# Kernel optimization log

Hardware: AMD Instinct MI355X
Metric: run time of the kernel (lower is better)

## Reference

```python
import jax, jax.numpy as jnp
import numpy as np

N_NODES = 50000
N_EDGES = 800000
IN_CH = 128
OUT_CH = 64
H1, C1 = 8, 8            # conv1: heads=8, out=8, concat -> 64
H2, C2 = 1, OUT_CH       # conv2: heads=1, out=64, concat=False
NEG_SLOPE = 0.2


def gat_conv(x, src, dst, W, att_src, att_dst, bias, heads, ch, concat):
    """PyG GATConv (self loops assumed already appended to src/dst).
    x: [N, F_in], W: [F_in, heads*ch], att_*: [heads, ch], bias: [heads*ch] or [ch]."""
    N = x.shape[0]
    h = (x @ W).reshape(N, heads, ch)                       # [N,H,C]
    a_s = jnp.einsum('nhc,hc->nh', h, att_src)              # [N,H]
    a_d = jnp.einsum('nhc,hc->nh', h, att_dst)              # [N,H]
    e = jax.nn.leaky_relu(a_s[src] + a_d[dst], NEG_SLOPE)   # [E,H]
    # segment softmax over incoming edges of each destination node
    m = jax.ops.segment_max(e, dst, num_segments=N)         # [N,H]
    ex = jnp.exp(e - m[dst])
    s = jax.ops.segment_sum(ex, dst, num_segments=N)        # [N,H]
    alpha = ex / (s[dst] + 1e-16)                           # [E,H]
    out = jax.ops.segment_sum(h[src] * alpha[:, :, None], dst, num_segments=N)  # [N,H,C]
    out = out.reshape(N, heads * ch) if concat else out.mean(axis=1)
    return out + bias


def setup_inputs() -> dict:
    key = jax.random.key(0)
    ks = jax.random.split(key, 12)
    glorot = lambda k, shape: jax.random.normal(k, shape, jnp.float32) * np.sqrt(2.0 / (shape[0] + shape[-1]))
    x = jax.random.normal(ks[0], (N_NODES, IN_CH), jnp.float32)
    edge_index = jax.random.randint(ks[1], (2, N_EDGES), 0, N_NODES, jnp.int64 if jax.config.read('jax_enable_x64') else jnp.int32).astype(jnp.int32)
    W1 = glorot(ks[2], (IN_CH, H1 * C1))
    att_src1 = glorot(ks[3], (H1, C1))
    att_dst1 = glorot(ks[4], (H1, C1))
    b1 = jnp.zeros((H1 * C1,), jnp.float32)
    W2 = glorot(ks[5], (H1 * C1, H2 * C2))
    att_src2 = glorot(ks[6], (H2, C2))
    att_dst2 = glorot(ks[7], (H2, C2))
    b2 = jnp.zeros((C2,), jnp.float32)
    return {"x": x, "edge_index": edge_index, "W1": W1, "att_src1": att_src1,
            "att_dst1": att_dst1, "b1": b1, "W2": W2, "att_src2": att_src2,
            "att_dst2": att_dst2, "b2": b2}


def reference(x, edge_index, W1, att_src1, att_dst1, b1, W2, att_src2, att_dst2, b2):
    N = x.shape[0]
    loops = jnp.arange(N, dtype=edge_index.dtype)
    src = jnp.concatenate([edge_index[0], loops])  # add_self_loops=True (PyG default)
    dst = jnp.concatenate([edge_index[1], loops])
    h = gat_conv(x, src, dst, W1, att_src1, att_dst1, b1, H1, C1, concat=True)
    h = jax.nn.elu(h)
    # F.dropout(training=self.training): identity in eval mode
    out = gat_conv(h, src, dst, W2, att_src2, att_dst2, b2, H2, C2, concat=False)
    return out
```

## Files before the change

kernel.cpp:

```cpp
#include <hip/hip_runtime.h>

#define NN 50000
#define NE 800000
#define NEG_SLOPE 0.2f

__device__ __forceinline__ float lrelu(float v) { return v > 0.f ? v : NEG_SLOPE * v; }
__device__ __forceinline__ unsigned short f2bf(float f) {
    unsigned u = __float_as_uint(f);
    return (unsigned short)((u + 0x7FFFu + ((u >> 16) & 1u)) >> 16);
}
__device__ __forceinline__ float rlane(float v, int l) {
    return __int_as_float(__builtin_amdgcn_readlane(__float_as_int(v), l));
}

__global__ __launch_bounds__(256) void setup(const float* __restrict__ W1,
                                             const float* __restrict__ W2,
                                             const float* __restrict__ as2,
                                             const float* __restrict__ ad2,
                                             int4* __restrict__ deg4,
                                             int* __restrict__ gcursor,
                                             float* __restrict__ W1S,
                                             float* __restrict__ W2S,
                                             float* __restrict__ w_as2,
                                             float* __restrict__ w_ad2) {
    int gid = blockIdx.x * 256 + threadIdx.x;
    if (gid < 12500) deg4[gid] = make_int4(0, 0, 0, 0);
    if (gid == 0) *gcursor = 0;
    if (gid < 8192) {
        int k = gid >> 6, c = gid & 63;
        W1S[((k >> 2) * 64 + c) * 4 + (k & 3)] = W1[k * 64 + c];
    } else if (gid < 12288) {
        int t = gid - 8192;
        int k = t >> 6, c = t & 63;
        W2S[((k >> 2) * 64 + c) * 4 + (k & 3)] = W2[k * 64 + c];
    }
    if (gid < 64) {
        float s = 0.f;
        for (int c = 0; c < 64; ++c) s += W2[gid * 64 + c] * as2[c];
        w_as2[gid] = s;
    } else if (gid < 128) {
        int k = gid - 64;
        float s = 0.f;
        for (int c = 0; c < 64; ++c) s += W2[k * 64 + c] * ad2[c];
        w_ad2[k] = s;
    }
}

__global__ __launch_bounds__(256) void hist_gemm1(const int* __restrict__ ei,
                                                  int* __restrict__ deg,
                                                  int* __restrict__ rank,
                                                  const float* __restrict__ x,
                                                  const float* __restrict__ W1S,
                                                  const float* __restrict__ att_s,
                                                  const float* __restrict__ att_d,
                                                  unsigned short* __restrict__ h1b,
                                                  float* __restrict__ a_s,
                                                  float2* __restrict__ nd1) {
    if (blockIdx.x < 3125) {
        int e = blockIdx.x * 256 + threadIdx.x;
        if (e < NE) rank[e] = atomicAdd(&deg[ei[NE + e]], 1);
        return;
    }
    int lane = threadIdx.x & 63;
    int wv   = __builtin_amdgcn_readfirstlane(threadIdx.x >> 6);
    int n0   = (blockIdx.x - 3125) * 16 + wv * 4;
    const float* __restrict__ xr = x + (size_t)n0 * 128;
    const float4* __restrict__ wp = (const float4*)W1S;
    float4 acc = {0.f, 0.f, 0.f, 0.f};
#pragma unroll 4
    for (int k4 = 0; k4 < 32; ++k4) {
        float4 w = wp[k4 * 64 + lane];
        const float* xk = xr + k4 * 4;
        acc.x += xk[0]   * w.x + xk[1]   * w.y + xk[2]   * w.z + xk[3]   * w.w;
        acc.y += xk[128] * w.x + xk[129] * w.y + xk[130] * w.z + xk[131] * w.w;
        acc.z += xk[256] * w.x + xk[257] * w.y + xk[258] * w.z + xk[259] * w.w;
        acc.w += xk[384] * w.x + xk[385] * w.y + xk[386] * w.z + xk[387] * w.w;
    }
    float as_l = att_s[lane], ad_l = att_d[lane];
    float av[4] = {acc.x, acc.y, acc.z, acc.w};
#pragma unroll
    for (int r = 0; r < 4; ++r) {
        float a = av[r];
        h1b[(size_t)(n0 + r) * 64 + lane] = f2bf(a);
        float ps = a * as_l, pd = a * ad_l;
        ps += __shfl_xor(ps, 1, 64); pd += __shfl_xor(pd, 1, 64);
        ps += __shfl_xor(ps, 2, 64); pd += __shfl_xor(pd, 2, 64);
        ps += __shfl_xor(ps, 4, 64); pd += __shfl_xor(pd, 4, 64);
        if ((lane & 7) == 0) {
            int h = lane >> 3;
            a_s[(n0 + r) * 8 + h] = ps;
            nd1[(n0 + r) * 8 + h] = make_float2(pd, lrelu(ps + pd));
        }
    }
}

__global__ __launch_bounds__(256) void scanA(const int* __restrict__ deg,
                                             int* __restrict__ offs,
                                             int* __restrict__ gcursor) {
    __shared__ int tmp[256];
    __shared__ int base;
    int i = blockIdx.x * 256 + threadIdx.x;
    int v = (i < NN) ? deg[i] : 0;
    tmp[threadIdx.x] = v;
    __syncthreads();
    for (int o = 1; o < 256; o <<= 1) {
        int t = (threadIdx.x >= o) ? tmp[threadIdx.x - o] : 0;
        __syncthreads();
        tmp[threadIdx.x] += t;
        __syncthreads();
    }
    if (threadIdx.x == 255) base = atomicAdd(gcursor, tmp[255]);
    __syncthreads();
    if (i < NN) offs[i] = base + tmp[threadIdx.x] - v;
}

__global__ void scatter(const int* __restrict__ ei, const int* __restrict__ rank,
                        const int* __restrict__ offs, int* __restrict__ srclist) {
    int e = blockIdx.x * blockDim.x + threadIdx.x;
    if (e < NE) {
        int d = ei[NE + e];
        srclist[offs[d] + rank[e]] = ei[e];
    }
}

__global__ __launch_bounds__(256) void agg1(const int* __restrict__ srclist,
                                            const int* __restrict__ offs,
                                            const int* __restrict__ degv,
                                            const float* __restrict__ a_s,
                                            const float2* __restrict__ nd1,
                                            const unsigned short* __restrict__ h1b,
                                            const float* __restrict__ b1,
                                            const float* __restrict__ w_as2,
                                            const float* __restrict__ w_ad2,
                                            unsigned short* __restrict__ xhb,
                                            float* __restrict__ a_s2,
                                            float2* __restrict__ nd2) {
    int wv   = threadIdx.x >> 6;
    int lane = threadIdx.x & 63;
    int d    = blockIdx.x * 4 + wv;
    int base = offs[d], dg = degv[d];
    int sub  = lane >> 3, hch = lane & 7;
    float2 nd = nd1[d * 8 + hch];
    float acc0 = 0.f, acc1 = 0.f, acc2 = 0.f, acc3 = 0.f;
    float acc4 = 0.f, acc5 = 0.f, acc6 = 0.f, acc7 = 0.f;
    float sm = 0.f;
    int k = sub;
    int s0 = 0, s1 = 0;
    float as0 = 0.f;
    uint4 hv0 = make_uint4(0, 0, 0, 0);
    if (k < dg)     s0 = srclist[base + k];
    if (k + 8 < dg) s1 = srclist[base + k + 8];
    if (k < dg) {
        as0 = a_s[s0 * 8 + hch];
        hv0 = *(const uint4*)&h1b[(size_t)s0 * 64 + hch * 8];
    }
    for (; k < dg; k += 8) {
        int   s2  = (k + 16 < dg) ? srclist[base + k + 16] : 0;
        float as1 = 0.f;
        uint4 hv1 = make_uint4(0, 0, 0, 0);
        if (k + 8 < dg) {
            as1 = a_s[s1 * 8 + hch];
            hv1 = *(const uint4*)&h1b[(size_t)s1 * 64 + hch * 8];
        }
        float ex = __expf(lrelu(as0 + nd.x) - nd.y);
        acc0 += __uint_as_float(hv0.x << 16)          * ex;
        acc1 += __uint_as_float(hv0.x & 0xffff0000u)  * ex;
        acc2 += __uint_as_float(hv0.y << 16)          * ex;
        acc3 += __uint_as_float(hv0.y & 0xffff0000u)  * ex;
        acc4 += __uint_as_float(hv0.z << 16)          * ex;
        acc5 += __uint_as_float(hv0.z & 0xffff0000u)  * ex;
        acc6 += __uint_as_float(hv0.w << 16)          * ex;
        acc7 += __uint_as_float(hv0.w & 0xffff0000u)  * ex;
        sm += ex;
        s0 = s1; s1 = s2; as0 = as1; hv0 = hv1;
    }
    if (sub == 0) {
        uint4 hv = *(const uint4*)&h1b[(size_t)d * 64 + hch * 8];
        acc0 += __uint_as_float(hv.x << 16);
        acc1 += __uint_as_float(hv.x & 0xffff0000u);
        acc2 += __uint_as_float(hv.y << 16);
        acc3 += __uint_as_float(hv.y & 0xffff0000u);
        acc4 += __uint_as_float(hv.z << 16);
        acc5 += __uint_as_float(hv.z & 0xffff0000u);
        acc6 += __uint_as_float(hv.w << 16);
        acc7 += __uint_as_float(hv.w & 0xffff0000u);
        sm += 1.f;
    }
#pragma unroll
    for (int m = 8; m < 64; m <<= 1) {
        acc0 += __shfl_xor(acc0, m, 64); acc1 += __shfl_xor(acc1, m, 64);
        acc2 += __shfl_xor(acc2, m, 64); acc3 += __shfl_xor(acc3, m, 64);
        acc4 += __shfl_xor(acc4, m, 64); acc5 += __shfl_xor(acc5, m, 64);
        acc6 += __shfl_xor(acc6, m, 64); acc7 += __shfl_xor(acc7, m, 64);
        sm   += __shfl_xor(sm, m, 64);
    }
    float inv = 1.f / sm;
    int li = (lane & 7) * 8;
    float4 bl = *(const float4*)&b1[li];
    float4 bh = *(const float4*)&b1[li + 4];
    float4 lo, hi;
    lo.x = acc0 * inv + bl.x; lo.x = lo.x > 0.f ? lo.x : expm1f(lo.x);
    lo.y = acc1 * inv + bl.y; lo.y = lo.y > 0.f ? lo.y : expm1f(lo.y);
    lo.z = acc2 * inv + bl.z; lo.z = lo.z > 0.f ? lo.z : expm1f(lo.z);
    lo.w = acc3 * inv + bl.w; lo.w = lo.w > 0.f ? lo.w : expm1f(lo.w);
    hi.x = acc4 * inv + bh.x; hi.x = hi.x > 0.f ? hi.x : expm1f(hi.x);
    hi.y = acc5 * inv + bh.y; hi.y = hi.y > 0.f ? hi.y : expm1f(hi.y);
    hi.z = acc6 * inv + bh.z; hi.z = hi.z > 0.f ? hi.z : expm1f(hi.z);
    hi.w = acc7 * inv + bh.w; hi.w = hi.w > 0.f ? hi.w : expm1f(hi.w);
    if (lane < 8) {
        uint4 pk;
        pk.x = ((unsigned)f2bf(lo.y) << 16) | f2bf(lo.x);
        pk.y = ((unsigned)f2bf(lo.w) << 16) | f2bf(lo.z);
        pk.z = ((unsigned)f2bf(hi.y) << 16) | f2bf(hi.x);
        pk.w = ((unsigned)f2bf(hi.w) << 16) | f2bf(hi.z);
        *(uint4*)&xhb[(size_t)d * 64 + lane * 8] = pk;
    }
    float4 s0v = *(const float4*)&w_as2[li], s1v = *(const float4*)&w_as2[li + 4];
    float4 d0v = *(const float4*)&w_ad2[li], d1v = *(const float4*)&w_ad2[li + 4];
    float ps = lo.x*s0v.x + lo.y*s0v.y + lo.z*s0v.z + lo.w*s0v.w
             + hi.x*s1v.x + hi.y*s1v.y + hi.z*s1v.z + hi.w*s1v.w;
    float pd = lo.x*d0v.x + lo.y*d0v.y + lo.z*d0v.z + lo.w*d0v.w
             + hi.x*d1v.x + hi.y*d1v.y + hi.z*d1v.z + hi.w*d1v.w;
    ps += __shfl_xor(ps, 1, 64); pd += __shfl_xor(pd, 1, 64);
    ps += __shfl_xor(ps, 2, 64); pd += __shfl_xor(pd, 2, 64);
    ps += __shfl_xor(ps, 4, 64); pd += __shfl_xor(pd, 4, 64);
    if (lane == 0) {
        a_s2[d] = ps;
        nd2[d]  = make_float2(pd, lrelu(ps + pd));
    }
}

__global__ __launch_bounds__(256) void agg2(const int* __restrict__ srclist,
                                            const int* __restrict__ offs,
                                            const int* __restrict__ degv,
                                            const float* __restrict__ a_s2,
                                            const float2* __restrict__ nd2,
                                            const unsigned short* __restrict__ xhb,
                                            const float* __restrict__ W2S,
                                            const float* __restrict__ b2,
                                            float* __restrict__ out) {
    int wv   = threadIdx.x >> 6;
    int lane = threadIdx.x & 63;
    int d    = blockIdx.x * 4 + wv;
    int base = offs[d], dg = degv[d];
    int sub  = lane >> 3, hch = lane & 7;
    float2 nd = nd2[d];
    float acc0 = 0.f, acc1 = 0.f, acc2 = 0.f, acc3 = 0.f;
    float acc4 = 0.f, acc5 = 0.f, acc6 = 0.f, acc7 = 0.f;
    float sm = 0.f;
    int k = sub;
    int s0 = 0, s1 = 0;
    float as0 = 0.f;
    uint4 hv0 = make_uint4(0, 0, 0, 0);
    if (k < dg)     s0 = srclist[base + k];
    if (k + 8 < dg) s1 = srclist[base + k + 8];
    if (k < dg) {
        as0 = a_s2[s0];
        hv0 = *(const uint4*)&xhb[(size_t)s0 * 64 + hch * 8];
    }
    for (; k < dg; k += 8) {
        int   s2  = (k + 16 < dg) ? srclist[base + k + 16] : 0;
        float as1 = 0.f;
        uint4 hv1 = make_uint4(0, 0, 0, 0);
        if (k + 8 < dg) {
            as1 = a_s2[s1];
            hv1 = *(const uint4*)&xhb[(size_t)s1 * 64 + hch * 8];
        }
        float ex = __expf(lrelu(as0 + nd.x) - nd.y);
        acc0 += __uint_as_float(hv0.x << 16)          * ex;
        acc1 += __uint_as_float(hv0.x & 0xffff0000u)  * ex;
        acc2 += __uint_as_float(hv0.y << 16)          * ex;
        acc3 += __uint_as_float(hv0.y & 0xffff0000u)  * ex;
        acc4 += __uint_as_float(hv0.z << 16)          * ex;
        acc5 += __uint_as_float(hv0.z & 0xffff0000u)  * ex;
        acc6 += __uint_as_float(hv0.w << 16)          * ex;
        acc7 += __uint_as_float(hv0.w & 0xffff0000u)  * ex;
        sm += ex;
        s0 = s1; s1 = s2; as0 = as1; hv0 = hv1;
    }
    if (sub == 0) {
        uint4 hv = *(const uint4*)&xhb[(size_t)d * 64 + hch * 8];
        acc0 += __uint_as_float(hv.x << 16);
        acc1 += __uint_as_float(hv.x & 0xffff0000u);
        acc2 += __uint_as_float(hv.y << 16);
        acc3 += __uint_as_float(hv.y & 0xffff0000u);
        acc4 += __uint_as_float(hv.z << 16);
        acc5 += __uint_as_float(hv.z & 0xffff0000u);
        acc6 += __uint_as_float(hv.w << 16);
        acc7 += __uint_as_float(hv.w & 0xffff0000u);
        sm += 1.f;
    }
#pragma unroll
    for (int m = 8; m < 64; m <<= 1) {
        acc0 += __shfl_xor(acc0, m, 64); acc1 += __shfl_xor(acc1, m, 64);
        acc2 += __shfl_xor(acc2, m, 64); acc3 += __shfl_xor(acc3, m, 64);
        acc4 += __shfl_xor(acc4, m, 64); acc5 += __shfl_xor(acc5, m, 64);
        acc6 += __shfl_xor(acc6, m, 64); acc7 += __shfl_xor(acc7, m, 64);
        sm   += __shfl_xor(sm, m, 64);
    }
    float inv = 1.f / sm;
    float t0 = acc0 * inv, t1 = acc1 * inv, t2 = acc2 * inv, t3 = acc3 * inv;
    float t4 = acc4 * inv, t5 = acc5 * inv, t6 = acc6 * inv, t7 = acc7 * inv;
    const float4* wp = (const float4*)W2S;
    float o = 0.f;
#pragma unroll
    for (int k4 = 0; k4 < 16; ++k4) {
        float4 w = wp[k4 * 64 + lane];
        int j = k4 >> 1;
        if (k4 & 1)
            o += rlane(t4, j) * w.x + rlane(t5, j) * w.y + rlane(t6, j) * w.z + rlane(t7, j) * w.w;
        else
            o += rlane(t0, j) * w.x + rlane(t1, j) * w.y + rlane(t2, j) * w.z + rlane(t3, j) * w.w;
    }
    out[(size_t)d * 64 + lane] = o + b2[lane];
}

extern "C" void kernel_launch(void* const* d_in, const int* in_sizes, int n_in,
                              void* d_out, int out_size, void* d_ws, size_t ws_size,
                              hipStream_t stream) {
    const float* x   = (const float*)d_in[0];
    const int*   ei  = (const int*)d_in[1];
    const float* W1  = (const float*)d_in[2];
    const float* as1 = (const float*)d_in[3];
    const float* ad1 = (const float*)d_in[4];
    const float* b1  = (const float*)d_in[5];
    const float* W2  = (const float*)d_in[6];
    const float* as2 = (const float*)d_in[7];
    const float* ad2 = (const float*)d_in[8];
    const float* b2  = (const float*)d_in[9];
    float* out = (float*)d_out;

    float* ws = (float*)d_ws;
    unsigned short* h1b = (unsigned short*)ws;
    unsigned short* xhb = (unsigned short*)(ws + 1600000);
    float*  a_s1 = ws + 3200000;
    float2* nd1  = (float2*)(ws + 3600000);
    float*  a_s2 = ws + 4400000;
    float2* nd2  = (float2*)(ws + 4450000);
    int* deg     = (int*)(ws + 4550000);
    int* offs    = deg + 50000;
    int* gcursor = offs + 50000;
    int* rank    = gcursor + 64;
    int* srclist = rank + 800000;
    float* W1S   = (float*)(srclist + 800000);
    float* W2S   = W1S + 8192;
    float* w_as2 = W2S + 4096;
    float* w_ad2 = w_as2 + 64;

    setup<<<49, 256, 0, stream>>>(W1, W2, as2, ad2, (int4*)deg, gcursor,
                                  W1S, W2S, w_as2, w_ad2);
    hist_gemm1<<<6250, 256, 0, stream>>>(ei, deg, rank, x, W1S, as1, ad1,
                                         h1b, a_s1, nd1);
    scanA<<<196, 256, 0, stream>>>(deg, offs, gcursor);
    scatter<<<3125, 256, 0, stream>>>(ei, rank, offs, srclist);

    agg1<<<12500, 256, 0, stream>>>(srclist, offs, deg, a_s1, nd1, h1b, b1,
                                    w_as2, w_ad2, xhb, a_s2, nd2);
    agg2<<<12500, 256, 0, stream>>>(srclist, offs, deg, a_s2, nd2, xhb, W2S, b2, out);
}
```

Before: 160.4 us.

## Split histogram out of GEMM and fuse CSR scatter with layer-1 GEMM

Moves the degree histogram into its own kernel that handles four strided edges per thread, and merges the CSR scatter into the layer-1 GEMM kernel. The scatter and GEMM now run as different block ranges of one launch, with each scatter thread also handling four edges. The aim is to cut per-thread launch and scheduling overhead on the small atomic and scatter passes and let the scatter overlap the GEMM. In exchange the GEMM no longer overlaps the histogram atomics, so the histogram now runs alone before the scan.

```diff
diff --git a/kernel.cpp b/kernel.cpp
--- a/kernel.cpp
+++ b/kernel.cpp
@@ -3,6 +3,7 @@
 #define NN 50000
 #define NE 800000
 #define NEG_SLOPE 0.2f
+#define S4 200192
 
 __device__ __forceinline__ float lrelu(float v) { return v > 0.f ? v : NEG_SLOPE * v; }
 __device__ __forceinline__ unsigned short f2bf(float f) {
@@ -46,24 +47,77 @@
     }
 }
 
-__global__ __launch_bounds__(256) void hist_gemm1(const int* __restrict__ ei,
-                                                  int* __restrict__ deg,
-                                                  int* __restrict__ rank,
-                                                  const float* __restrict__ x,
-                                                  const float* __restrict__ W1S,
-                                                  const float* __restrict__ att_s,
-                                                  const float* __restrict__ att_d,
-                                                  unsigned short* __restrict__ h1b,
-                                                  float* __restrict__ a_s,
-                                                  float2* __restrict__ nd1) {
-    if (blockIdx.x < 3125) {
-        int e = blockIdx.x * 256 + threadIdx.x;
-        if (e < NE) rank[e] = atomicAdd(&deg[ei[NE + e]], 1);
+__global__ __launch_bounds__(256) void hist4(const int* __restrict__ ei,
+                                             int* __restrict__ deg,
+                                             int* __restrict__ rank) {
+    int tid = blockIdx.x * 256 + threadIdx.x;
+    int e0 = tid, e1 = tid + S4, e2 = tid + 2 * S4, e3 = tid + 3 * S4;
+    bool p3 = e3 < NE;
+    int d0 = ei[NE + e0];
+    int d1 = ei[NE + e1];
+    int d2 = ei[NE + e2];
+    int d3 = p3 ? ei[NE + e3] : 0;
+    int r0 = atomicAdd(&deg[d0], 1);
+    int r1 = atomicAdd(&deg[d1], 1);
+    int r2 = atomicAdd(&deg[d2], 1);
+    int r3 = p3 ? atomicAdd(&deg[d3], 1) : 0;
+    rank[e0] = r0;
+    rank[e1] = r1;
+    rank[e2] = r2;
+    if (p3) rank[e3] = r3;
+}
+
+__global__ __launch_bounds__(256) void scanA(const int* __restrict__ deg,
+                                             int* __restrict__ offs,
+                                             int* __restrict__ gcursor) {
+    __shared__ int tmp[256];
+    __shared__ int base;
+    int i = blockIdx.x * 256 + threadIdx.x;
+    int v = (i < NN) ? deg[i] : 0;
+    tmp[threadIdx.x] = v;
+    __syncthreads();
+    for (int o = 1; o < 256; o <<= 1) {
+        int t = (threadIdx.x >= o) ? tmp[threadIdx.x - o] : 0;
+        __syncthreads();
+        tmp[threadIdx.x] += t;
+        __syncthreads();
+    }
+    if (threadIdx.x == 255) base = atomicAdd(gcursor, tmp[255]);
+    __syncthreads();
+    if (i < NN) offs[i] = base + tmp[threadIdx.x] - v;
+}
+
+__global__ __launch_bounds__(256) void scatter_gemm1(const int* __restrict__ ei,
+                                                     const int* __restrict__ rank,
+                                                     const int* __restrict__ offs,
+                                                     int* __restrict__ srclist,
+                                                     const float* __restrict__ x,
+                                                     const float* __restrict__ W1S,
+                                                     const float* __restrict__ att_s,
+                                                     const float* __restrict__ att_d,
+                                                     unsigned short* __restrict__ h1b,
+                                                     float* __restrict__ a_s,
+                                                     float2* __restrict__ nd1) {
+    if (blockIdx.x < 782) {
+        int tid = blockIdx.x * 256 + threadIdx.x;
+        int e0 = tid, e1 = tid + S4, e2 = tid + 2 * S4, e3 = tid + 3 * S4;
+        bool p3 = e3 < NE;
+        int s0 = ei[e0], d0 = ei[NE + e0], r0 = rank[e0];
+        int s1 = ei[e1], d1 = ei[NE + e1], r1 = rank[e1];
+        int s2 = ei[e2], d2 = ei[NE + e2], r2 = rank[e2];
+        int s3 = 0, d3 = 0, r3 = 0;
+        if (p3) { s3 = ei[e3]; d3 = ei[NE + e3]; r3 = rank[e3]; }
+        int o0 = offs[d0], o1 = offs[d1], o2 = offs[d2];
+        int o3 = p3 ? offs[d3] : 0;
+        srclist[o0 + r0] = s0;
+        srclist[o1 + r1] = s1;
+        srclist[o2 + r2] = s2;
+        if (p3) srclist[o3 + r3] = s3;
         return;
     }
     int lane = threadIdx.x & 63;
     int wv   = __builtin_amdgcn_readfirstlane(threadIdx.x >> 6);
-    int n0   = (blockIdx.x - 3125) * 16 + wv * 4;
+    int n0   = (blockIdx.x - 782) * 16 + wv * 4;
     const float* __restrict__ xr = x + (size_t)n0 * 128;
     const float4* __restrict__ wp = (const float4*)W1S;
     float4 acc = {0.f, 0.f, 0.f, 0.f};
@@ -91,35 +145,6 @@
             a_s[(n0 + r) * 8 + h] = ps;
             nd1[(n0 + r) * 8 + h] = make_float2(pd, lrelu(ps + pd));
         }
-    }
-}
-
-__global__ __launch_bounds__(256) void scanA(const int* __restrict__ deg,
-                                             int* __restrict__ offs,
-                                             int* __restrict__ gcursor) {
-    __shared__ int tmp[256];
-    __shared__ int base;
-    int i = blockIdx.x * 256 + threadIdx.x;
-    int v = (i < NN) ? deg[i] : 0;
-    tmp[threadIdx.x] = v;
-    __syncthreads();
-    for (int o = 1; o < 256; o <<= 1) {
-        int t = (threadIdx.x >= o) ? tmp[threadIdx.x - o] : 0;
-        __syncthreads();
-        tmp[threadIdx.x] += t;
-        __syncthreads();
-    }
-    if (threadIdx.x == 255) base = atomicAdd(gcursor, tmp[255]);
-    __syncthreads();
-    if (i < NN) offs[i] = base + tmp[threadIdx.x] - v;
-}
-
-__global__ void scatter(const int* __restrict__ ei, const int* __restrict__ rank,
-                        const int* __restrict__ offs, int* __restrict__ srclist) {
-    int e = blockIdx.x * blockDim.x + threadIdx.x;
-    if (e < NE) {
-        int d = ei[NE + e];
-        srclist[offs[d] + rank[e]] = ei[e];
     }
 }
 
@@ -349,10 +374,10 @@
 
     setup<<<49, 256, 0, stream>>>(W1, W2, as2, ad2, (int4*)deg, gcursor,
                                   W1S, W2S, w_as2, w_ad2);
-    hist_gemm1<<<6250, 256, 0, stream>>>(ei, deg, rank, x, W1S, as1, ad1,
-                                         h1b, a_s1, nd1);
+    hist4<<<782, 256, 0, stream>>>(ei, deg, rank);
     scanA<<<196, 256, 0, stream>>>(deg, offs, gcursor);
-    scatter<<<3125, 256, 0, stream>>>(ei, rank, offs, srclist);
+    scatter_gemm1<<<3907, 256, 0, stream>>>(ei, rank, offs, srclist, x, W1S,
+                                            as1, ad1, h1b, a_s1, nd1);
 
     agg1<<<12500, 256, 0, stream>>>(srclist, offs, deg, a_s1, nd1, h1b, b1,
                                     w_as2, w_ad2, xhb, a_s2, nd2);
```

After: 159.6 us. Within noise of the previous version (-0.5%).
